# Performance work log

Hardware: AMD Instinct MI355X
Metric: run time of the kernel (lower is better)

Reference implementation:

```python
import jax, jax.numpy as jnp
import numpy as np

B, S, D = 8, 1024, 1024
H, DH = 16, 64  # n_heads, d_head; D == H*DH


def setup_inputs() -> dict:
    key = jax.random.key(0)
    ks = jax.random.split(key, 7)
    scale = 1.0 / np.sqrt(DH)
    return {
        "images": jax.random.normal(ks[0], (B, S, D), dtype=jnp.float32),
        "Wq": jax.random.normal(ks[1], (H, DH, DH), dtype=jnp.float32) * scale,
        "bq": jax.random.normal(ks[2], (H, DH), dtype=jnp.float32) * scale,
        "Wk": jax.random.normal(ks[3], (H, DH, DH), dtype=jnp.float32) * scale,
        "bk": jax.random.normal(ks[4], (H, DH), dtype=jnp.float32) * scale,
        "Wv": jax.random.normal(ks[5], (H, DH, DH), dtype=jnp.float32) * scale,
        "bv": jax.random.normal(ks[6], (H, DH), dtype=jnp.float32) * scale,
    }


def reference(images, Wq, bq, Wk, bk, Wv, bv):
    Bn, Sn, Dn = images.shape
    x = images.reshape(Bn, Sn, H, DH)  # split hidden dim into per-head slices
    # torch Linear: y = x @ W.T + b, per head -> einsum over input dim d
    q = jnp.einsum("bshd,hod->bsho", x, Wq) + bq  # [B,S,H,DH]
    k = jnp.einsum("bshd,hod->bsho", x, Wk) + bk
    v = jnp.einsum("bshd,hod->bsho", x, Wv) + bv
    scores = jnp.einsum("bqhd,bkhd->bhqk", q, k) / jnp.sqrt(jnp.asarray(DH, x.dtype))
    attn = jax.nn.softmax(scores, axis=-1)  # [B,H,S,S]
    out = jnp.einsum("bhqk,bkhd->bqhd", attn, v)  # [B,S,H,DH]
    return out.reshape(Bn, Sn, Dn)  # hstack across heads == reshape back
```

## Files before the change

### kernel.cpp

```cpp
#include <hip/hip_runtime.h>
#include <hip/hip_bf16.h>

#define B_ 8
#define S_ 1024
#define D_ 1024
#define H_ 16
#define DH_ 64

typedef __attribute__((ext_vector_type(8))) short short8;
typedef __attribute__((ext_vector_type(8))) unsigned short ushort8;
typedef __attribute__((ext_vector_type(4))) unsigned short us4;
typedef __attribute__((ext_vector_type(4))) unsigned int uint4v;
typedef __attribute__((ext_vector_type(4))) float f32x4;

#define QSCALE 0.18033688011112042f

static __device__ __forceinline__ unsigned short f2bf(float f) {
    union { float f; unsigned u; } v; v.f = f;
    unsigned r = v.u + 0x7fffu + ((v.u >> 16) & 1u);
    return (unsigned short)(r >> 16);
}

static __device__ __forceinline__ void stage8(const float* __restrict__ src, unsigned short* dst) {
    float4 a = *reinterpret_cast<const float4*>(src);
    float4 b = *reinterpret_cast<const float4*>(src + 4);
    ushort8 r;
    r[0] = f2bf(a.x); r[1] = f2bf(a.y); r[2] = f2bf(a.z); r[3] = f2bf(a.w);
    r[4] = f2bf(b.x); r[5] = f2bf(b.y); r[6] = f2bf(b.z); r[7] = f2bf(b.w);
    *reinterpret_cast<ushort8*>(dst) = r;
}

static __device__ __forceinline__ unsigned int cvtpk(float a, float b) {
    unsigned int r;
    asm("v_cvt_pk_bf16_f32 %0, %1, %2" : "=v"(r) : "v"(a), "v"(b));
    return r;
}

static __device__ __forceinline__ void gll16(const void* g, void* l) {
    __builtin_amdgcn_global_load_lds(
        (const __attribute__((address_space(1))) unsigned int*)g,
        (__attribute__((address_space(3))) unsigned int*)l,
        16, 0, 0);
}

__global__ __launch_bounds__(256) void qkv_proj(
    const float* __restrict__ x,
    const float* __restrict__ Wq, const float* __restrict__ bq,
    const float* __restrict__ Wk, const float* __restrict__ bk,
    const float* __restrict__ Wv, const float* __restrict__ bv,
    unsigned short* __restrict__ qo, unsigned short* __restrict__ ko,
    unsigned short* __restrict__ vo)
{
    const int bid   = blockIdx.x;
    const int stile = bid & 15;
    const int h     = (bid >> 4) & (H_ - 1);
    const int b     = bid >> 8;
    const int tid   = threadIdx.x;
    const int lane  = tid & 63;
    const int wave  = tid >> 6;
    const int lr    = lane & 15;
    const int lk    = lane >> 4;

    __shared__ __align__(16) unsigned short xs[64][72];
    __shared__ __align__(16) unsigned short wsh[3][64][72];

    {
        int row = tid >> 2;
        int col = (tid & 3) * 16;
        const float* src = x + ((size_t)(b * S_ + stile * 64 + row)) * D_ + h * DH_ + col;
        stage8(src,     &xs[row][col]);
        stage8(src + 8, &xs[row][col + 8]);
        const float* wsrc[3] = { Wq + h * DH_ * DH_, Wk + h * DH_ * DH_, Wv + h * DH_ * DH_ };
        #pragma unroll
        for (int p = 0; p < 3; ++p) {
            const float* s = wsrc[p] + row * DH_ + col;
            stage8(s,     &wsh[p][row][col]);
            stage8(s + 8, &wsh[p][row][col + 8]);
        }
    }
    __syncthreads();

    short8 a[2];
    #pragma unroll
    for (int kk = 0; kk < 2; ++kk)
        a[kk] = *reinterpret_cast<const short8*>(&xs[wave * 16 + lr][8 * lk + 32 * kk]);

    f32x4 acc[3][4];
    #pragma unroll
    for (int p = 0; p < 3; ++p)
        #pragma unroll
        for (int n = 0; n < 4; ++n)
            acc[p][n] = (f32x4){0.f, 0.f, 0.f, 0.f};

    #pragma unroll
    for (int p = 0; p < 3; ++p)
        #pragma unroll
        for (int kk = 0; kk < 2; ++kk)
            #pragma unroll
            for (int n = 0; n < 4; ++n) {
                short8 bf = *reinterpret_cast<const short8*>(&wsh[p][lr + 16 * n][8 * lk + 32 * kk]);
                acc[p][n] = __builtin_amdgcn_mfma_f32_16x16x32_bf16(a[kk], bf, acc[p][n], 0, 0, 0);
            }

    size_t base = ((size_t)(b * H_ + h) * S_ + stile * 64 + wave * 16) * DH_;
    #pragma unroll
    for (int p = 0; p < 2; ++p) {
        const float* bias = p ? (bk + h * DH_) : (bq + h * DH_);
        unsigned short* op = p ? ko : qo;
        #pragma unroll
        for (int n = 0; n < 4; ++n) {
            int col = lr + 16 * n;
            float bb = bias[col];
            #pragma unroll
            for (int r = 0; r < 4; ++r) {
                float val = acc[p][n][r] + bb;
                if (p == 0) val *= QSCALE;
                op[base + (size_t)(4 * lk + r) * DH_ + col] = f2bf(val);
            }
        }
    }
    {
        size_t vbase = (size_t)(b * H_ + h) * DH_ * S_;
        int s0 = stile * 64 + wave * 16 + 4 * lk;
        #pragma unroll
        for (int n = 0; n < 4; ++n) {
            int dh = lr + 16 * n;
            float bb = bv[h * DH_ + dh];
            us4 w;
            #pragma unroll
            for (int r = 0; r < 4; ++r) w[r] = f2bf(acc[2][n][r] + bb);
            *reinterpret_cast<us4*>(vo + vbase + (size_t)dh * S_ + s0) = w;
        }
    }
}

__global__ __launch_bounds__(256, 2) void attn_fwd(
    const unsigned short* __restrict__ q,
    const unsigned short* __restrict__ k,
    const unsigned short* __restrict__ vt,
    float* __restrict__ out)
{
    const int bid   = (blockIdx.x & 7) * 64 + (blockIdx.x >> 3);
    const int qtile = bid & 3;
    const int h     = (bid >> 2) & (H_ - 1);
    const int b     = bid >> 6;
    const int tid   = threadIdx.x;
    const int lane  = tid & 63;
    const int wave  = tid >> 6;
    const int lr    = lane & 15;
    const int lk    = lane >> 4;

    __shared__ __align__(16) unsigned short ks[3][64][64];
    __shared__ __align__(16) unsigned short vs[3][64][64];

    const size_t bh = (size_t)(b * H_ + h) * S_ * DH_;

    short8 qf[4][2];
    #pragma unroll
    for (int g = 0; g < 4; ++g) {
        const unsigned short* qp = q + bh + (size_t)(qtile * 256 + wave * 64 + 16 * g + lr) * DH_;
        #pragma unroll
        for (int kk = 0; kk < 2; ++kk)
            qf[g][kk] = *reinterpret_cast<const short8*>(qp + 8 * lk + 32 * kk);
    }

    short8 ones;
    {
        ushort8 ou;
        #pragma unroll
        for (int j = 0; j < 8; ++j) ou[j] = 0x3F80;
        ones = __builtin_bit_cast(short8, ou);
    }

    const int rp0 = 16 * wave + (lane >> 3);
    const int rp1 = rp0 + 8;
    const int c   = lane & 7;
    const int gk0 = (rp0 & 0x23) | ((rp0 & 0x10) >> 2) | ((rp0 & 0x0C) << 1);
    const int gk1 = (rp1 & 0x23) | ((rp1 & 0x10) >> 2) | ((rp1 & 0x0C) << 1);
    const size_t kofs0 = (size_t)gk0 * DH_ + (c ^ (rp0 & 7)) * 8;
    const size_t kofs1 = (size_t)gk1 * DH_ + (c ^ (rp1 & 7)) * 8;
    const size_t vofs0 = (size_t)rp0 * S_ + (c ^ (rp0 & 7)) * 8;
    const size_t vofs1 = (size_t)rp1 * S_ + (c ^ (rp1 & 7)) * 8;
    const unsigned short* kb = k + bh;
    const unsigned short* vb = vt + bh;

    gll16(kb + kofs0, &ks[0][16 * wave][0]);
    gll16(kb + kofs1, &ks[0][16 * wave + 8][0]);
    gll16(vb + vofs0, &vs[0][16 * wave][0]);
    gll16(vb + vofs1, &vs[0][16 * wave + 8][0]);
    {
        const unsigned short* kt = kb + (size_t)64 * DH_;
        const unsigned short* vtb = vb + 64;
        gll16(kt + kofs0, &ks[1][16 * wave][0]);
        gll16(kt + kofs1, &ks[1][16 * wave + 8][0]);
        gll16(vtb + vofs0, &vs[1][16 * wave][0]);
        gll16(vtb + vofs1, &vs[1][16 * wave + 8][0]);
    }
    asm volatile("s_waitcnt vmcnt(4)" ::: "memory");
    __builtin_amdgcn_sched_barrier(0);
    __builtin_amdgcn_s_barrier();
    __builtin_amdgcn_sched_barrier(0);

    f32x4 acc[4][4], accl[4];
    #pragma unroll
    for (int g = 0; g < 4; ++g) {
        #pragma unroll
        for (int n = 0; n < 4; ++n) acc[g][n] = (f32x4){0.f, 0.f, 0.f, 0.f};
        accl[g] = (f32x4){0.f, 0.f, 0.f, 0.f};
    }

    const int rx = lr & 7;
    const int NT = S_ / 64;
    for (int t = 0; t < NT; ++t) {
        const int bc = t % 3;

        if (t + 2 < NT) {
            const int bn = (t + 2) % 3;
            const unsigned short* kt = kb + (size_t)(t + 2) * 64 * DH_;
            const unsigned short* vtb = vb + (size_t)(t + 2) * 64;
            gll16(kt + kofs0, &ks[bn][16 * wave][0]);
            gll16(kt + kofs1, &ks[bn][16 * wave + 8][0]);
            gll16(vtb + vofs0, &vs[bn][16 * wave][0]);
            gll16(vtb + vofs1, &vs[bn][16 * wave + 8][0]);
        }

        short8 ka[8], va[8];
        #pragma unroll
        for (int i = 0; i < 8; ++i) {
            const int kk = i >> 2, n = i & 3;
            const int col = ((lk + 4 * kk) ^ rx) * 8;
            ka[i] = *reinterpret_cast<const short8*>(&ks[bc][16 * n + lr][col]);
            va[i] = *reinterpret_cast<const short8*>(&vs[bc][16 * n + lr][col]);
        }

        #pragma unroll
        for (int g = 0; g < 4; ++g) {
            f32x4 st[4];
            #pragma unroll
            for (int n = 0; n < 4; ++n) st[n] = (f32x4){0.f, 0.f, 0.f, 0.f};
            __builtin_amdgcn_s_setprio(1);
            #pragma unroll
            for (int kk = 0; kk < 2; ++kk)
                #pragma unroll
                for (int n = 0; n < 4; ++n)
                    st[n] = __builtin_amdgcn_mfma_f32_16x16x32_bf16(ka[4 * kk + n], qf[g][kk], st[n], 0, 0, 0);
            __builtin_amdgcn_s_setprio(0);

            #pragma unroll
            for (int n = 0; n < 4; ++n)
                #pragma unroll
                for (int r = 0; r < 4; ++r)
                    st[n][r] = __builtin_amdgcn_exp2f(st[n][r]);

            short8 pa[2];
            #pragma unroll
            for (int kk = 0; kk < 2; ++kk) {
                uint4v w4;
                w4[0] = cvtpk(st[2 * kk][0],     st[2 * kk][1]);
                w4[1] = cvtpk(st[2 * kk][2],     st[2 * kk][3]);
                w4[2] = cvtpk(st[2 * kk + 1][0], st[2 * kk + 1][1]);
                w4[3] = cvtpk(st[2 * kk + 1][2], st[2 * kk + 1][3]);
                pa[kk] = __builtin_bit_cast(short8, w4);
            }

            __builtin_amdgcn_s_setprio(1);
            #pragma unroll
            for (int kk = 0; kk < 2; ++kk) {
                #pragma unroll
                for (int n = 0; n < 4; ++n)
                    acc[g][n] = __builtin_amdgcn_mfma_f32_16x16x32_bf16(va[4 * kk + n], pa[kk], acc[g][n], 0, 0, 0);
                accl[g] = __builtin_amdgcn_mfma_f32_16x16x32_bf16(ones, pa[kk], accl[g], 0, 0, 0);
            }
            __builtin_amdgcn_s_setprio(0);
        }

        if (t + 1 < NT) {
            if (t + 2 < NT) asm volatile("s_waitcnt vmcnt(4)" ::: "memory");
            else            asm volatile("s_waitcnt vmcnt(0)" ::: "memory");
            __builtin_amdgcn_sched_barrier(0);
            __builtin_amdgcn_s_barrier();
            __builtin_amdgcn_sched_barrier(0);
        }
    }

    #pragma unroll
    for (int g = 0; g < 4; ++g) {
        const float inv = 1.f / accl[g][0];
        const int qrow = qtile * 256 + wave * 64 + 16 * g + lr;
        float* op = out + (size_t)(b * S_ + qrow) * D_ + h * DH_;
        #pragma unroll
        for (int n = 0; n < 4; ++n) {
            float4 o;
            o.x = acc[g][n][0] * inv; o.y = acc[g][n][1] * inv;
            o.z = acc[g][n][2] * inv; o.w = acc[g][n][3] * inv;
            *reinterpret_cast<float4*>(op + 16 * n + 4 * lk) = o;
        }
    }
}

extern "C" void kernel_launch(void* const* d_in, const int* in_sizes, int n_in,
                              void* d_out, int out_size, void* d_ws, size_t ws_size,
                              hipStream_t stream) {
    const float* x  = (const float*)d_in[0];
    const float* Wq = (const float*)d_in[1];
    const float* bq = (const float*)d_in[2];
    const float* Wk = (const float*)d_in[3];
    const float* bk = (const float*)d_in[4];
    const float* Wv = (const float*)d_in[5];
    const float* bv = (const float*)d_in[6];
    float* out = (float*)d_out;

    unsigned short* qw = (unsigned short*)d_ws;
    size_t per = (size_t)B_ * H_ * S_ * DH_;
    unsigned short* kw = qw + per;
    unsigned short* vw = kw + per;

    qkv_proj<<<dim3(B_ * H_ * (S_ / 64)), 256, 0, stream>>>(x, Wq, bq, Wk, bk, Wv, bv, qw, kw, vw);
    attn_fwd<<<dim3(B_ * H_ * (S_ / 256)), 256, 0, stream>>>(qw, kw, vw, out);
}
```

Before: 62.56 us.

## Switch attention MFMAs from 16x16x32 to 32x32x16 bf16 tiles

Rewrites the attention kernel's QK^T and PV matrix products to use 32x32x16 bf16 MFMA instructions instead of 16x16x32. Q fragments, K/V LDS reads, the permuted K row mapping, the accumulator layout and the output store are all remapped to the 32-row tiling. Larger MFMA tiles raise arithmetic per LDS fragment load and cut the number of instructions issued. In exchange, register pressure goes up because all score tiles for a 64-key block are now live at once.

```diff
diff --git a/kernel.cpp b/kernel.cpp
--- a/kernel.cpp
+++ b/kernel.cpp
@@ -12,6 +12,7 @@
 typedef __attribute__((ext_vector_type(4))) unsigned short us4;
 typedef __attribute__((ext_vector_type(4))) unsigned int uint4v;
 typedef __attribute__((ext_vector_type(4))) float f32x4;
+typedef __attribute__((ext_vector_type(16))) float f32x16;
 
 #define QSCALE 0.18033688011112042f
 
@@ -147,21 +148,21 @@
     const int tid   = threadIdx.x;
     const int lane  = tid & 63;
     const int wave  = tid >> 6;
-    const int lr    = lane & 15;
-    const int lk    = lane >> 4;
+    const int lq    = lane & 31;
+    const int hi    = lane >> 5;
 
     __shared__ __align__(16) unsigned short ks[3][64][64];
     __shared__ __align__(16) unsigned short vs[3][64][64];
 
     const size_t bh = (size_t)(b * H_ + h) * S_ * DH_;
 
-    short8 qf[4][2];
-    #pragma unroll
-    for (int g = 0; g < 4; ++g) {
-        const unsigned short* qp = q + bh + (size_t)(qtile * 256 + wave * 64 + 16 * g + lr) * DH_;
-        #pragma unroll
-        for (int kk = 0; kk < 2; ++kk)
-            qf[g][kk] = *reinterpret_cast<const short8*>(qp + 8 * lk + 32 * kk);
+    short8 qf[2][4];
+    #pragma unroll
+    for (int qb = 0; qb < 2; ++qb) {
+        const unsigned short* qp = q + bh + (size_t)(qtile * 256 + wave * 64 + 32 * qb + lq) * DH_;
+        #pragma unroll
+        for (int kkq = 0; kkq < 4; ++kkq)
+            qf[qb][kkq] = *reinterpret_cast<const short8*>(qp + 16 * kkq + 8 * hi);
     }
 
     short8 ones;
@@ -175,8 +176,8 @@
     const int rp0 = 16 * wave + (lane >> 3);
     const int rp1 = rp0 + 8;
     const int c   = lane & 7;
-    const int gk0 = (rp0 & 0x23) | ((rp0 & 0x10) >> 2) | ((rp0 & 0x0C) << 1);
-    const int gk1 = (rp1 & 0x23) | ((rp1 & 0x10) >> 2) | ((rp1 & 0x0C) << 1);
+    const int gk0 = (rp0 & 0x23) | ((rp0 & 0x10) >> 2) | ((rp0 & 4) << 1) | ((rp0 & 8) << 1);
+    const int gk1 = (rp1 & 0x23) | ((rp1 & 0x10) >> 2) | ((rp1 & 4) << 1) | ((rp1 & 8) << 1);
     const size_t kofs0 = (size_t)gk0 * DH_ + (c ^ (rp0 & 7)) * 8;
     const size_t kofs1 = (size_t)gk1 * DH_ + (c ^ (rp1 & 7)) * 8;
     const size_t vofs0 = (size_t)rp0 * S_ + (c ^ (rp0 & 7)) * 8;
@@ -201,15 +202,18 @@
     __builtin_amdgcn_s_barrier();
     __builtin_amdgcn_sched_barrier(0);
 
-    f32x4 acc[4][4], accl[4];
-    #pragma unroll
-    for (int g = 0; g < 4; ++g) {
-        #pragma unroll
-        for (int n = 0; n < 4; ++n) acc[g][n] = (f32x4){0.f, 0.f, 0.f, 0.f};
-        accl[g] = (f32x4){0.f, 0.f, 0.f, 0.f};
-    }
-
-    const int rx = lr & 7;
+    f32x16 acc[2][2], accl[2];
+    #pragma unroll
+    for (int qb = 0; qb < 2; ++qb) {
+        #pragma unroll
+        for (int db = 0; db < 2; ++db)
+            #pragma unroll
+            for (int e = 0; e < 16; ++e) acc[qb][db][e] = 0.f;
+        #pragma unroll
+        for (int e = 0; e < 16; ++e) accl[qb][e] = 0.f;
+    }
+
+    const int rxk = lq & 7;
     const int NT = S_ / 64;
     for (int t = 0; t < NT; ++t) {
         const int bc = t % 3;
@@ -224,55 +228,62 @@
             gll16(vtb + vofs1, &vs[bn][16 * wave + 8][0]);
         }
 
-        short8 ka[8], va[8];
-        #pragma unroll
-        for (int i = 0; i < 8; ++i) {
-            const int kk = i >> 2, n = i & 3;
-            const int col = ((lk + 4 * kk) ^ rx) * 8;
-            ka[i] = *reinterpret_cast<const short8*>(&ks[bc][16 * n + lr][col]);
-            va[i] = *reinterpret_cast<const short8*>(&vs[bc][16 * n + lr][col]);
-        }
-
-        #pragma unroll
-        for (int g = 0; g < 4; ++g) {
-            f32x4 st[4];
-            #pragma unroll
-            for (int n = 0; n < 4; ++n) st[n] = (f32x4){0.f, 0.f, 0.f, 0.f};
-            __builtin_amdgcn_s_setprio(1);
-            #pragma unroll
-            for (int kk = 0; kk < 2; ++kk)
+        f32x16 st[2][2];
+        #pragma unroll
+        for (int qb = 0; qb < 2; ++qb)
+            #pragma unroll
+            for (int B = 0; B < 2; ++B)
                 #pragma unroll
-                for (int n = 0; n < 4; ++n)
-                    st[n] = __builtin_amdgcn_mfma_f32_16x16x32_bf16(ka[4 * kk + n], qf[g][kk], st[n], 0, 0, 0);
-            __builtin_amdgcn_s_setprio(0);
-
-            #pragma unroll
-            for (int n = 0; n < 4; ++n)
+                for (int e = 0; e < 16; ++e) st[qb][B][e] = 0.f;
+        __builtin_amdgcn_s_setprio(1);
+        #pragma unroll
+        for (int kkq = 0; kkq < 4; ++kkq)
+            #pragma unroll
+            for (int B = 0; B < 2; ++B) {
+                short8 ka = *reinterpret_cast<const short8*>(
+                    &ks[bc][32 * B + lq][((2 * kkq + hi) ^ rxk) * 8]);
+                st[0][B] = __builtin_amdgcn_mfma_f32_32x32x16_bf16(ka, qf[0][kkq], st[0][B], 0, 0, 0);
+                st[1][B] = __builtin_amdgcn_mfma_f32_32x32x16_bf16(ka, qf[1][kkq], st[1][B], 0, 0, 0);
+            }
+        __builtin_amdgcn_s_setprio(0);
+
+        #pragma unroll
+        for (int qb = 0; qb < 2; ++qb)
+            #pragma unroll
+            for (int B = 0; B < 2; ++B)
                 #pragma unroll
-                for (int r = 0; r < 4; ++r)
-                    st[n][r] = __builtin_amdgcn_exp2f(st[n][r]);
-
-            short8 pa[2];
-            #pragma unroll
-            for (int kk = 0; kk < 2; ++kk) {
-                uint4v w4;
-                w4[0] = cvtpk(st[2 * kk][0],     st[2 * kk][1]);
-                w4[1] = cvtpk(st[2 * kk][2],     st[2 * kk][3]);
-                w4[2] = cvtpk(st[2 * kk + 1][0], st[2 * kk + 1][1]);
-                w4[3] = cvtpk(st[2 * kk + 1][2], st[2 * kk + 1][3]);
-                pa[kk] = __builtin_bit_cast(short8, w4);
-            }
-
-            __builtin_amdgcn_s_setprio(1);
-            #pragma unroll
-            for (int kk = 0; kk < 2; ++kk) {
+                for (int e = 0; e < 16; ++e)
+                    st[qb][B][e] = __builtin_amdgcn_exp2f(st[qb][B][e]);
+
+        short8 pa[2][4];
+        #pragma unroll
+        for (int qb = 0; qb < 2; ++qb)
+            #pragma unroll
+            for (int B = 0; B < 2; ++B)
                 #pragma unroll
-                for (int n = 0; n < 4; ++n)
-                    acc[g][n] = __builtin_amdgcn_mfma_f32_16x16x32_bf16(va[4 * kk + n], pa[kk], acc[g][n], 0, 0, 0);
-                accl[g] = __builtin_amdgcn_mfma_f32_16x16x32_bf16(ones, pa[kk], accl[g], 0, 0, 0);
-            }
-            __builtin_amdgcn_s_setprio(0);
-        }
+                for (int kkl = 0; kkl < 2; ++kkl) {
+                    uint4v w4;
+                    w4[0] = cvtpk(st[qb][B][4 * kkl + 0],  st[qb][B][4 * kkl + 1]);
+                    w4[1] = cvtpk(st[qb][B][4 * kkl + 2],  st[qb][B][4 * kkl + 3]);
+                    w4[2] = cvtpk(st[qb][B][4 * kkl + 8],  st[qb][B][4 * kkl + 9]);
+                    w4[3] = cvtpk(st[qb][B][4 * kkl + 10], st[qb][B][4 * kkl + 11]);
+                    pa[qb][2 * B + kkl] = __builtin_bit_cast(short8, w4);
+                }
+
+        __builtin_amdgcn_s_setprio(1);
+        #pragma unroll
+        for (int kk = 0; kk < 4; ++kk) {
+            #pragma unroll
+            for (int db = 0; db < 2; ++db) {
+                short8 va = *reinterpret_cast<const short8*>(
+                    &vs[bc][32 * db + lq][((2 * kk + hi) ^ rxk) * 8]);
+                acc[0][db] = __builtin_amdgcn_mfma_f32_32x32x16_bf16(va, pa[0][kk], acc[0][db], 0, 0, 0);
+                acc[1][db] = __builtin_amdgcn_mfma_f32_32x32x16_bf16(va, pa[1][kk], acc[1][db], 0, 0, 0);
+            }
+            accl[0] = __builtin_amdgcn_mfma_f32_32x32x16_bf16(ones, pa[0][kk], accl[0], 0, 0, 0);
+            accl[1] = __builtin_amdgcn_mfma_f32_32x32x16_bf16(ones, pa[1][kk], accl[1], 0, 0, 0);
+        }
+        __builtin_amdgcn_s_setprio(0);
 
         if (t + 1 < NT) {
             if (t + 2 < NT) asm volatile("s_waitcnt vmcnt(4)" ::: "memory");
@@ -284,17 +295,21 @@
     }
 
     #pragma unroll
-    for (int g = 0; g < 4; ++g) {
-        const float inv = 1.f / accl[g][0];
-        const int qrow = qtile * 256 + wave * 64 + 16 * g + lr;
+    for (int qb = 0; qb < 2; ++qb) {
+        const float inv = 1.f / accl[qb][0];
+        const int qrow = qtile * 256 + wave * 64 + 32 * qb + lq;
         float* op = out + (size_t)(b * S_ + qrow) * D_ + h * DH_;
         #pragma unroll
-        for (int n = 0; n < 4; ++n) {
-            float4 o;
-            o.x = acc[g][n][0] * inv; o.y = acc[g][n][1] * inv;
-            o.z = acc[g][n][2] * inv; o.w = acc[g][n][3] * inv;
-            *reinterpret_cast<float4*>(op + 16 * n + 4 * lk) = o;
-        }
+        for (int db = 0; db < 2; ++db)
+            #pragma unroll
+            for (int m = 0; m < 4; ++m) {
+                float4 o;
+                o.x = acc[qb][db][4 * m + 0] * inv;
+                o.y = acc[qb][db][4 * m + 1] * inv;
+                o.z = acc[qb][db][4 * m + 2] * inv;
+                o.w = acc[qb][db][4 * m + 3] * inv;
+                *reinterpret_cast<float4*>(op + 32 * db + 8 * m + 4 * hi) = o;
+            }
     }
 }
 
```

Measured after the change: 68.73 us. 9.9% more time.
